# Kernel tuning notes

Hardware: AMD Instinct MI355X
Metric: run time of the kernel (lower is better)

The kernel has to match this reference:

```python
import jax, jax.numpy as jnp
import numpy as np

DM = 1024
H = 16
DEPTH = DM // H


def setup_inputs() -> dict:
    key = jax.random.key(0)
    ks = jax.random.split(key, 11)
    B, S = 2, 2048
    scale = 1.0 / np.sqrt(DM)
    inp = {
        "Q": jax.random.normal(ks[0], (B, S, DM), dtype=jnp.float32),
        "K": jax.random.normal(ks[1], (B, S, DM), dtype=jnp.float32),
        "V": jax.random.normal(ks[2], (B, S, DM), dtype=jnp.float32),
        "Wq": jax.random.normal(ks[3], (DM, DM), dtype=jnp.float32) * scale,
        "bq": jnp.zeros((DM,), dtype=jnp.float32),
        "Wk": jax.random.normal(ks[4], (DM, DM), dtype=jnp.float32) * scale,
        "bk": jnp.zeros((DM,), dtype=jnp.float32),
        "Wv": jax.random.normal(ks[5], (DM, DM), dtype=jnp.float32) * scale,
        "bv": jnp.zeros((DM,), dtype=jnp.float32),
        "Wo": jax.random.normal(ks[6], (DM, DM), dtype=jnp.float32) * scale,
        "bo": jnp.zeros((DM,), dtype=jnp.float32),
    }
    return inp


def _split_heads(x, B):
    # [B, S, DM] -> [B, H, S, DEPTH]
    return x.reshape(B, -1, H, DEPTH).transpose(0, 2, 1, 3)


def reference(Q, K, V, Wq, bq, Wk, bk, Wv, bv, Wo, bo):
    B = Q.shape[0]
    q = _split_heads(Q @ Wq + bq, B)  # [B,H,S,D]
    k = _split_heads(K @ Wk + bk, B)
    v = _split_heads(V @ Wv + bv, B)
    logits = jnp.einsum("bhqd,bhkd->bhqk", q, k) / jnp.sqrt(
        jnp.asarray(DEPTH, dtype=q.dtype))
    weights = jax.nn.softmax(logits, axis=-1)  # [B,H,S,S]
    attn = jnp.einsum("bhqk,bhkd->bhqd", weights, v)
    concat = attn.transpose(0, 2, 1, 3).reshape(B, -1, DM)
    output = concat @ Wo + bo
    return output, weights
```

## Files before the change

### kernel.cpp

```cpp
#include <hip/hip_runtime.h>
#include <hip/hip_fp16.h>
#include <stdint.h>
#include <stddef.h>

typedef _Float16 f16;
typedef _Float16 f16x8 __attribute__((ext_vector_type(8)));
typedef _Float16 f16x4 __attribute__((ext_vector_type(4)));
typedef float    f32x4 __attribute__((ext_vector_type(4)));

#define NB  2
#define NS  2048
#define NDM 1024
#define NH  16
#define ND  64
#define NM  4096

__global__ __launch_bounds__(256) void cvt_x_kernel(const float* __restrict__ q,
                                                    const float* __restrict__ k,
                                                    const float* __restrict__ v,
                                                    f16* __restrict__ xh)
{
    const float* src = (blockIdx.y == 0) ? q : (blockIdx.y == 1) ? k : v;
    f16* dst = xh + (size_t)blockIdx.y * ((size_t)NM * NDM);
    size_t i = ((size_t)blockIdx.x * 256 + threadIdx.x) * 8;
    float4 a = *(const float4*)(src + i);
    float4 b = *(const float4*)(src + i + 4);
    f16x8 o;
    o[0] = (f16)a.x; o[1] = (f16)a.y; o[2] = (f16)a.z; o[3] = (f16)a.w;
    o[4] = (f16)b.x; o[5] = (f16)b.y; o[6] = (f16)b.z; o[7] = (f16)b.w;
    *(f16x8*)(dst + i) = o;
}

__global__ __launch_bounds__(256) void transp_w_kernel(const float* __restrict__ w0,
                                                       const float* __restrict__ w1,
                                                       const float* __restrict__ w2,
                                                       const float* __restrict__ w3,
                                                       f16* __restrict__ wt)
{
    __shared__ float t[64][65];
    const int z = blockIdx.z;
    const float* src = (z==0)?w0:(z==1)?w1:(z==2)?w2:w3;
    f16* dst = wt + (size_t)z * ((size_t)NDM * NDM);
    const int k0 = blockIdx.y * 64, n0 = blockIdx.x * 64;
    const int c = threadIdx.x & 63, r4 = threadIdx.x >> 6;
    #pragma unroll
    for (int i = 0; i < 16; ++i) {
        int r = i*4 + r4;
        t[r][c] = src[(size_t)(k0 + r) * NDM + n0 + c];
    }
    __syncthreads();
    #pragma unroll
    for (int i = 0; i < 16; ++i) {
        int n = i*4 + r4;
        dst[(size_t)(n0 + n) * NDM + k0 + c] = (f16)t[c][n];
    }
}

template<int MODE>
__device__ __forceinline__ void gemm128(const f16* __restrict__ A,
                                        const f16* __restrict__ Bw,
                                        const float* __restrict__ bias,
                                        void* __restrict__ outp,
                                        f16* __restrict__ AsB, f16* __restrict__ BsB)
{
    const int tid  = threadIdx.x;
    const int lane = tid & 63;
    const int wid  = tid >> 6;
    const int wr = wid >> 1, wc = wid & 1;
    const int m0 = blockIdx.y * 128, n0 = blockIdx.x * 128;
    const int K = 1024;

    const int r0 = tid >> 2;
    const int s0 = (tid & 3) * 8;
    const f16* Arow0 = A  + (size_t)(m0 + r0)      * K + s0;
    const f16* Arow1 = A  + (size_t)(m0 + r0 + 64) * K + s0;
    const f16* Brow0 = Bw + (size_t)(n0 + r0)      * K + s0;
    const f16* Brow1 = Bw + (size_t)(n0 + r0 + 64) * K + s0;
    const int lds0 = r0*32 + s0;
    const int lds1 = (r0+64)*32 + s0;

    f16x8 ra0 = *(const f16x8*)(Arow0);
    f16x8 ra1 = *(const f16x8*)(Arow1);
    f16x8 rb0 = *(const f16x8*)(Brow0);
    f16x8 rb1 = *(const f16x8*)(Brow1);
    *(f16x8*)(AsB + lds0) = ra0; *(f16x8*)(AsB + lds1) = ra1;
    *(f16x8*)(BsB + lds0) = rb0; *(f16x8*)(BsB + lds1) = rb1;

    f32x4 acc[4][4];
    #pragma unroll
    for (int i = 0; i < 4; ++i)
        #pragma unroll
        for (int j = 0; j < 4; ++j) {
            f32x4 z4 = {0.f, 0.f, 0.f, 0.f};
            acc[i][j] = z4;
        }

    const int arow = wr*64 + (lane & 15);
    const int brow = wc*64 + (lane & 15);
    const int kc   = (lane >> 4) * 8;

    int cur = 0;
    for (int s = 0; s < 32; ++s) {
        const bool more = (s + 1 < 32);
        if (more) {
            const int kk = (s + 1) * 32;
            ra0 = *(const f16x8*)(Arow0 + kk); ra1 = *(const f16x8*)(Arow1 + kk);
            rb0 = *(const f16x8*)(Brow0 + kk); rb1 = *(const f16x8*)(Brow1 + kk);
        }
        __syncthreads();
        {
            f16x8 af[4], bf[4];
            f16* Asc = AsB + cur*4096;
            f16* Bsc = BsB + cur*4096;
            #pragma unroll
            for (int rt = 0; rt < 4; ++rt) af[rt] = *(const f16x8*)(Asc + (arow + rt*16)*32 + kc);
            #pragma unroll
            for (int ct = 0; ct < 4; ++ct) bf[ct] = *(const f16x8*)(Bsc + (brow + ct*16)*32 + kc);
            #pragma unroll
            for (int rt = 0; rt < 4; ++rt)
                #pragma unroll
                for (int ct = 0; ct < 4; ++ct)
                    acc[rt][ct] = __builtin_amdgcn_mfma_f32_16x16x32_f16(af[rt], bf[ct], acc[rt][ct], 0, 0, 0);
        }
        __syncthreads();
        if (more) {
            f16* Asn = AsB + (cur^1)*4096;
            f16* Bsn = BsB + (cur^1)*4096;
            *(f16x8*)(Asn + lds0) = ra0; *(f16x8*)(Asn + lds1) = ra1;
            *(f16x8*)(Bsn + lds0) = rb0; *(f16x8*)(Bsn + lds1) = rb1;
        }
        cur ^= 1;
    }

    #pragma unroll
    for (int rt = 0; rt < 4; ++rt) {
        const int mb = m0 + wr*64 + rt*16 + ((lane >> 4) << 2);
        #pragma unroll
        for (int ct = 0; ct < 4; ++ct) {
            const int n = n0 + wc*64 + ct*16 + (lane & 15);
            const float bn = bias[n];
            if (MODE == 0 || MODE == 1) {
                f16* dst = (f16*)outp;
                const float sc = (MODE == 0) ? 0.125f : 1.0f;
                #pragma unroll
                for (int j = 0; j < 4; ++j) {
                    const int m = mb + j;
                    const float v = (acc[rt][ct][j] + bn) * sc;
                    dst[(size_t)((m >> 11)*16 + (n >> 6))*131072 + (size_t)(m & 2047)*64 + (n & 63)] = (f16)v;
                }
            } else if (MODE == 2) {
                f16* dst = (f16*)outp;
                f16x4 o;
                #pragma unroll
                for (int j = 0; j < 4; ++j) o[j] = (f16)(acc[rt][ct][j] + bn);
                *(f16x4*)(dst + (size_t)((mb >> 11)*16 + (n >> 6))*131072 + (size_t)(n & 63)*2048 + (mb & 2047)) = o;
            } else {
                float* dst = (float*)outp;
                #pragma unroll
                for (int j = 0; j < 4; ++j) {
                    const int m = mb + j;
                    dst[(size_t)m * NDM + n] = acc[rt][ct][j] + bn;
                }
            }
        }
    }
}

__global__ __launch_bounds__(256) void proj_kernel(const f16* __restrict__ xh, const f16* __restrict__ wt,
                                                   const float* __restrict__ bq, const float* __restrict__ bk,
                                                   const float* __restrict__ bv,
                                                   f16* __restrict__ qh, f16* __restrict__ kh, f16* __restrict__ vh)
{
    __shared__ f16 AsS[2*4096];
    __shared__ f16 BsS[2*4096];
    const int z = blockIdx.z;
    const f16* A  = xh + (size_t)z * ((size_t)NM * NDM);
    const f16* Bw = wt + (size_t)z * ((size_t)NDM * NDM);
    if (z == 0)      gemm128<0>(A, Bw, bq, qh, AsS, BsS);
    else if (z == 1) gemm128<1>(A, Bw, bk, kh, AsS, BsS);
    else             gemm128<2>(A, Bw, bv, vh, AsS, BsS);
}

__global__ __launch_bounds__(256) void outproj_kernel(const f16* __restrict__ ah, const f16* __restrict__ wto,
                                                      const float* __restrict__ bo, float* __restrict__ out)
{
    __shared__ f16 AsS[2*4096];
    __shared__ f16 BsS[2*4096];
    gemm128<3>(ah, wto, bo, out, AsS, BsS);
}

__global__ __launch_bounds__(512) void attn_kernel(const f16* __restrict__ qh, const f16* __restrict__ kh,
                                                   const f16* __restrict__ vt, f16* __restrict__ ah,
                                                   float* __restrict__ wout)
{
    __shared__ f16   st[16 * 2056];
    __shared__ float scratch[2048];
    __shared__ float rinv[16];

    const int tid  = threadIdx.x;
    const int lane = tid & 63;
    const int wid  = tid >> 6;
    const int bh    = blockIdx.x >> 7;
    const int qbase = (blockIdx.x & 127) * 16;

    const f16* qp = qh + ((size_t)bh * NS + qbase) * 64;
    const f16* kp = kh + (size_t)bh * NS * 64;
    const f16* vp = vt + (size_t)bh * 64 * NS;

    const int l15 = lane & 15;
    const int g   = lane >> 4;

    const f16x8 qf0 = *(const f16x8*)(qp + l15*64 + g*8);
    const f16x8 qf1 = *(const f16x8*)(qp + l15*64 + 32 + g*8);

    float rs = 0.f;
    const f16* kbase = kp + (size_t)(wid*16 + l15) * 64 + g*8;
    f16* stw = st + l15*2056 + wid*16 + g*4;

    for (int t = 0; t < 16; ++t) {
        const f16* kb = kbase + (size_t)t * (128*64);
        f16x8 kf0 = *(const f16x8*)(kb);
        f16x8 kf1 = *(const f16x8*)(kb + 32);
        f32x4 a = {0.f, 0.f, 0.f, 0.f};
        a = __builtin_amdgcn_mfma_f32_16x16x32_f16(kf0, qf0, a, 0, 0, 0);
        a = __builtin_amdgcn_mfma_f32_16x16x32_f16(kf1, qf1, a, 0, 0, 0);
        f16x4 sv;
        #pragma unroll
        for (int j = 0; j < 4; ++j) {
            float e = __expf(a[j]);
            e = fminf(e, 60000.0f);
            rs += e;
            sv[j] = (f16)e;
        }
        *(f16x4*)(stw + t*128) = sv;
    }

    rs += __shfl_xor(rs, 16);
    rs += __shfl_xor(rs, 32);
    if (lane < 16) scratch[wid*16 + lane] = rs;
    __syncthreads();
    if (tid < 16) {
        float sum = 0.f;
        #pragma unroll
        for (int w = 0; w < 8; ++w) sum += scratch[w*16 + tid];
        rinv[tid] = 1.0f / sum;
    }
    __syncthreads();

    {
        const int r = tid >> 5, c = tid & 31;
        const float ri = rinv[r];
        const f16x4* srow = (const f16x4*)(st + r*2056);
        float* orow = wout + ((size_t)bh * NS + qbase + r) * NS;
        #pragma unroll
        for (int i = 0; i < 16; ++i) {
            f16x4 sv = srow[c + i*32];
            float4 o;
            o.x = (float)sv[0] * ri; o.y = (float)sv[1] * ri;
            o.z = (float)sv[2] * ri; o.w = (float)sv[3] * ri;
            *(float4*)(orow + (size_t)(c + i*32)*4) = o;
        }
    }

    {
        const int nt = wid & 3;
        const int khalf = wid >> 2;
        f32x4 acc = {0.f, 0.f, 0.f, 0.f};
        const f16* vb = vp + (size_t)(nt*16 + l15) * NS + khalf*1024 + g*8;
        const f16* sb = st + l15*2056 + khalf*1024 + g*8;
        #pragma unroll 4
        for (int ks = 0; ks < 32; ++ks) {
            f16x8 sf = *(const f16x8*)(sb + ks*32);
            f16x8 vf = *(const f16x8*)(vb + ks*32);
            acc = __builtin_amdgcn_mfma_f32_16x16x32_f16(sf, vf, acc, 0, 0, 0);
        }
        #pragma unroll
        for (int j = 0; j < 4; ++j)
            scratch[khalf*1024 + (g*4 + j)*64 + nt*16 + l15] = acc[j];
    }
    __syncthreads();

    {
        const int b = bh >> 4, hh = bh & 15;
        for (int idx = tid; idx < 1024; idx += 512) {
            const int r = idx >> 6, d = idx & 63;
            const float v = (scratch[r*64 + d] + scratch[1024 + r*64 + d]) * rinv[r];
            ah[((size_t)(b*NS + qbase + r)) * NDM + hh*64 + d] = (f16)v;
        }
    }
}

extern "C" void kernel_launch(void* const* d_in, const int* in_sizes, int n_in,
                              void* d_out, int out_size, void* d_ws, size_t ws_size,
                              hipStream_t stream)
{
    (void)in_sizes; (void)n_in; (void)out_size;
    const float* Q  = (const float*)d_in[0];
    const float* K  = (const float*)d_in[1];
    const float* V  = (const float*)d_in[2];
    const float* Wq = (const float*)d_in[3];
    const float* bq = (const float*)d_in[4];
    const float* Wk = (const float*)d_in[5];
    const float* bk = (const float*)d_in[6];
    const float* Wv = (const float*)d_in[7];
    const float* bv = (const float*)d_in[8];
    const float* Wo = (const float*)d_in[9];
    const float* bo = (const float*)d_in[10];

    if (ws_size < 67108864ull) return;

    f16* ws = (f16*)d_ws;
    f16* Xh = ws;
    f16* Wt = ws + 12582912;
    f16* qh = ws + 16777216;
    f16* kh = ws + 20971520;
    f16* vt = ws + 25165824;
    f16* ah = ws + 29360128;
    float* out  = (float*)d_out;
    float* wout = out + 4194304;

    cvt_x_kernel  <<<dim3(2048, 3, 1), dim3(256), 0, stream>>>(Q, K, V, Xh);
    transp_w_kernel<<<dim3(16, 16, 4), dim3(256), 0, stream>>>(Wq, Wk, Wv, Wo, Wt);
    proj_kernel   <<<dim3(8, 32, 3),  dim3(256), 0, stream>>>(Xh, Wt, bq, bk, bv, qh, kh, vt);
    attn_kernel   <<<dim3(4096),      dim3(512), 0, stream>>>(qh, kh, vt, ah, wout);
    outproj_kernel<<<dim3(8, 32, 1),  dim3(256), 0, stream>>>(ah, Wt + 3*1048576, bo, out);
}
```

Baseline: 389.1 us.

## Restructure attention as two-pass per-wave kernel with exp2 and XCD-aware block mapping

```diff
diff --git a/kernel.cpp b/kernel.cpp
--- a/kernel.cpp
+++ b/kernel.cpp
@@ -141,7 +141,7 @@
             const float bn = bias[n];
             if (MODE == 0 || MODE == 1) {
                 f16* dst = (f16*)outp;
-                const float sc = (MODE == 0) ? 0.125f : 1.0f;
+                const float sc = (MODE == 0) ? 0.125f * 1.44269504088896f : 1.0f;
                 #pragma unroll
                 for (int j = 0; j < 4; ++j) {
                     const int m = mb + j;
@@ -189,104 +189,100 @@
     gemm128<3>(ah, wto, bo, out, AsS, BsS);
 }
 
-__global__ __launch_bounds__(512) void attn_kernel(const f16* __restrict__ qh, const f16* __restrict__ kh,
-                                                   const f16* __restrict__ vt, f16* __restrict__ ah,
-                                                   float* __restrict__ wout)
-{
-    __shared__ f16   st[16 * 2056];
-    __shared__ float scratch[2048];
-    __shared__ float rinv[16];
+__global__ __launch_bounds__(512, 4) void attn_kernel(const f16* __restrict__ qh,
+                                                      const f16* __restrict__ kh,
+                                                      const f16* __restrict__ vt,
+                                                      f16* __restrict__ ah,
+                                                      float* __restrict__ wout)
+{
+    __shared__ __align__(16) f16 pbuf[8][16][40];
 
     const int tid  = threadIdx.x;
     const int lane = tid & 63;
     const int wid  = tid >> 6;
-    const int bh    = blockIdx.x >> 7;
-    const int qbase = (blockIdx.x & 127) * 16;
-
-    const f16* qp = qh + ((size_t)bh * NS + qbase) * 64;
+    const int l15  = lane & 15;
+    const int g    = lane >> 4;
+
+    const int xcd = blockIdx.x & 7;
+    const int jj  = blockIdx.x >> 3;
+    const int bh  = xcd * 4 + (jj & 3);
+    const int qrow = (jj >> 2) * 128 + wid * 16 + l15;
+
+    const f16* qp = qh + ((size_t)bh * NS + qrow) * 64;
     const f16* kp = kh + (size_t)bh * NS * 64;
     const f16* vp = vt + (size_t)bh * 64 * NS;
 
-    const int l15 = lane & 15;
-    const int g   = lane >> 4;
-
-    const f16x8 qf0 = *(const f16x8*)(qp + l15*64 + g*8);
-    const f16x8 qf1 = *(const f16x8*)(qp + l15*64 + 32 + g*8);
+    const f16x8 qf0 = *(const f16x8*)(qp + g*8);
+    const f16x8 qf1 = *(const f16x8*)(qp + 32 + g*8);
 
     float rs = 0.f;
-    const f16* kbase = kp + (size_t)(wid*16 + l15) * 64 + g*8;
-    f16* stw = st + l15*2056 + wid*16 + g*4;
-
-    for (int t = 0; t < 16; ++t) {
-        const f16* kb = kbase + (size_t)t * (128*64);
-        f16x8 kf0 = *(const f16x8*)(kb);
-        f16x8 kf1 = *(const f16x8*)(kb + 32);
-        f32x4 a = {0.f, 0.f, 0.f, 0.f};
-        a = __builtin_amdgcn_mfma_f32_16x16x32_f16(kf0, qf0, a, 0, 0, 0);
-        a = __builtin_amdgcn_mfma_f32_16x16x32_f16(kf1, qf1, a, 0, 0, 0);
-        f16x4 sv;
-        #pragma unroll
-        for (int j = 0; j < 4; ++j) {
-            float e = __expf(a[j]);
-            e = fminf(e, 60000.0f);
-            rs += e;
-            sv[j] = (f16)e;
-        }
-        *(f16x4*)(stw + t*128) = sv;
-    }
-
+    for (int t = 0; t < 64; ++t) {
+        const f16* ka = kp + (size_t)(t*32 + l15) * 64 + g*8;
+        f32x4 a = {0.f,0.f,0.f,0.f}, b = {0.f,0.f,0.f,0.f};
+        a = __builtin_amdgcn_mfma_f32_16x16x32_f16(*(const f16x8*)(ka),        qf0, a, 0,0,0);
+        a = __builtin_amdgcn_mfma_f32_16x16x32_f16(*(const f16x8*)(ka + 32),   qf1, a, 0,0,0);
+        b = __builtin_amdgcn_mfma_f32_16x16x32_f16(*(const f16x8*)(ka + 1024), qf0, b, 0,0,0);
+        b = __builtin_amdgcn_mfma_f32_16x16x32_f16(*(const f16x8*)(ka + 1056), qf1, b, 0,0,0);
+        #pragma unroll
+        for (int u = 0; u < 4; ++u)
+            rs += __builtin_amdgcn_exp2f(a[u]) + __builtin_amdgcn_exp2f(b[u]);
+    }
     rs += __shfl_xor(rs, 16);
     rs += __shfl_xor(rs, 32);
-    if (lane < 16) scratch[wid*16 + lane] = rs;
-    __syncthreads();
-    if (tid < 16) {
-        float sum = 0.f;
-        #pragma unroll
-        for (int w = 0; w < 8; ++w) sum += scratch[w*16 + tid];
-        rinv[tid] = 1.0f / sum;
-    }
-    __syncthreads();
+    const float ri = 1.0f / rs;
+
+    f32x4 acc0 = {0.f,0.f,0.f,0.f}, acc1 = acc0, acc2 = acc0, acc3 = acc0;
+    f16* pb = &pbuf[wid][0][0];
+    float* wr = wout + ((size_t)bh * NS + qrow) * NS;
+    const f16* vb0 = vp + (size_t)l15 * NS + g*8;
+
+    for (int t = 0; t < 64; ++t) {
+        const f16* ka = kp + (size_t)(t*32 + l15) * 64 + g*8;
+        f32x4 a = {0.f,0.f,0.f,0.f}, b = {0.f,0.f,0.f,0.f};
+        a = __builtin_amdgcn_mfma_f32_16x16x32_f16(*(const f16x8*)(ka),        qf0, a, 0,0,0);
+        a = __builtin_amdgcn_mfma_f32_16x16x32_f16(*(const f16x8*)(ka + 32),   qf1, a, 0,0,0);
+        b = __builtin_amdgcn_mfma_f32_16x16x32_f16(*(const f16x8*)(ka + 1024), qf0, b, 0,0,0);
+        b = __builtin_amdgcn_mfma_f32_16x16x32_f16(*(const f16x8*)(ka + 1056), qf1, b, 0,0,0);
+
+        f32x4 ea, eb; f16x4 pa, pc;
+        #pragma unroll
+        for (int u = 0; u < 4; ++u) {
+            ea[u] = __builtin_amdgcn_exp2f(a[u]); eb[u] = __builtin_amdgcn_exp2f(b[u]);
+            pa[u] = (f16)ea[u];    pc[u] = (f16)eb[u];
+        }
+        *(f16x4*)(pb + l15*40 + g*4)      = pa;
+        *(f16x4*)(pb + l15*40 + 16 + g*4) = pc;
+
+        f32x4 wa, wb;
+        #pragma unroll
+        for (int u = 0; u < 4; ++u) { wa[u] = ea[u]*ri; wb[u] = eb[u]*ri; }
+        __builtin_nontemporal_store(wa, (f32x4*)(wr + t*32 + g*4));
+        __builtin_nontemporal_store(wb, (f32x4*)(wr + t*32 + 16 + g*4));
+
+        f16x8 pf = *(const f16x8*)(pb + l15*40 + g*8);
+        const f16* vb = vb0 + t*32;
+        acc0 = __builtin_amdgcn_mfma_f32_16x16x32_f16(*(const f16x8*)(vb),           pf, acc0, 0,0,0);
+        acc1 = __builtin_amdgcn_mfma_f32_16x16x32_f16(*(const f16x8*)(vb + 16*NS),   pf, acc1, 0,0,0);
+        acc2 = __builtin_amdgcn_mfma_f32_16x16x32_f16(*(const f16x8*)(vb + 32*NS),   pf, acc2, 0,0,0);
+        acc3 = __builtin_amdgcn_mfma_f32_16x16x32_f16(*(const f16x8*)(vb + 48*NS),   pf, acc3, 0,0,0);
+    }
 
     {
-        const int r = tid >> 5, c = tid & 31;
-        const float ri = rinv[r];
-        const f16x4* srow = (const f16x4*)(st + r*2056);
-        float* orow = wout + ((size_t)bh * NS + qbase + r) * NS;
-        #pragma unroll
-        for (int i = 0; i < 16; ++i) {
-            f16x4 sv = srow[c + i*32];
-            float4 o;
-            o.x = (float)sv[0] * ri; o.y = (float)sv[1] * ri;
-            o.z = (float)sv[2] * ri; o.w = (float)sv[3] * ri;
-            *(float4*)(orow + (size_t)(c + i*32)*4) = o;
-        }
-    }
-
-    {
-        const int nt = wid & 3;
-        const int khalf = wid >> 2;
-        f32x4 acc = {0.f, 0.f, 0.f, 0.f};
-        const f16* vb = vp + (size_t)(nt*16 + l15) * NS + khalf*1024 + g*8;
-        const f16* sb = st + l15*2056 + khalf*1024 + g*8;
-        #pragma unroll 4
-        for (int ks = 0; ks < 32; ++ks) {
-            f16x8 sf = *(const f16x8*)(sb + ks*32);
-            f16x8 vf = *(const f16x8*)(vb + ks*32);
-            acc = __builtin_amdgcn_mfma_f32_16x16x32_f16(sf, vf, acc, 0, 0, 0);
-        }
-        #pragma unroll
-        for (int j = 0; j < 4; ++j)
-            scratch[khalf*1024 + (g*4 + j)*64 + nt*16 + l15] = acc[j];
-    }
-    __syncthreads();
-
-    {
-        const int b = bh >> 4, hh = bh & 15;
-        for (int idx = tid; idx < 1024; idx += 512) {
-            const int r = idx >> 6, d = idx & 63;
-            const float v = (scratch[r*64 + d] + scratch[1024 + r*64 + d]) * rinv[r];
-            ah[((size_t)(b*NS + qbase + r)) * NDM + hh*64 + d] = (f16)v;
-        }
+        const int bb = bh >> 4, hh = bh & 15;
+        f16* arow = ah + ((size_t)(bb*NS + qrow)) * NDM + hh*64 + g*4;
+        f16x4 o;
+        #pragma unroll
+        for (int u = 0; u < 4; ++u) o[u] = (f16)(acc0[u] * ri);
+        *(f16x4*)(arow) = o;
+        #pragma unroll
+        for (int u = 0; u < 4; ++u) o[u] = (f16)(acc1[u] * ri);
+        *(f16x4*)(arow + 16) = o;
+        #pragma unroll
+        for (int u = 0; u < 4; ++u) o[u] = (f16)(acc2[u] * ri);
+        *(f16x4*)(arow + 32) = o;
+        #pragma unroll
+        for (int u = 0; u < 4; ++u) o[u] = (f16)(acc3[u] * ri);
+        *(f16x4*)(arow + 48) = o;
     }
 }
 
@@ -322,6 +318,6 @@
     cvt_x_kernel  <<<dim3(2048, 3, 1), dim3(256), 0, stream>>>(Q, K, V, Xh);
     transp_w_kernel<<<dim3(16, 16, 4), dim3(256), 0, stream>>>(Wq, Wk, Wv, Wo, Wt);
     proj_kernel   <<<dim3(8, 32, 3),  dim3(256), 0, stream>>>(Xh, Wt, bq, bk, bv, qh, kh, vt);
-    attn_kernel   <<<dim3(4096),      dim3(512), 0, stream>>>(qh, kh, vt, ah, wout);
+    attn_kernel   <<<dim3(512),       dim3(512), 0, stream>>>(qh, kh, vt, ah, wout);
     outproj_kernel<<<dim3(8, 32, 1),  dim3(256), 0, stream>>>(ah, Wt + 3*1048576, bo, out);
 }
```

Result: slower. 447.3 us (+15.0%).
